# Kernel tuning notes

Measured on AMD Instinct MI355X. Metric: run time of the kernel, lower is better.

Reference implementation:

```python
import jax, jax.numpy as jnp
import numpy as np

N = 50000      # nodes
IN = 128       # in_channels
H = 2          # heads
C = 64         # hidden_channels (per head)
E = 800000     # edges (before self-loops)
OUT = 40       # out_channels
BN_EPS = 1e-5
NEG_SLOPE = 0.2  # PyG GATConv default


def _bn(x, g, b):
    # BatchNorm1d forward with batch statistics (training-mode math, biased var)
    mu = jnp.mean(x, axis=0)
    v = jnp.var(x, axis=0)
    return (x - mu) * jax.lax.rsqrt(v + BN_EPS) * g + b


def _gat_conv(x, src, dst, W, a_src, a_dst, bias, concat):
    n = x.shape[0]
    h = (x @ W).reshape(n, H, C)                      # [N,H,C] per-head projection
    al_s = jnp.einsum('nhc,hc->nh', h, a_src)         # [N,H]
    al_d = jnp.einsum('nhc,hc->nh', h, a_dst)
    e = jax.nn.leaky_relu(al_s[src] + al_d[dst], NEG_SLOPE)  # [E,H]
    # segment softmax over edges sharing the same destination
    m = jax.ops.segment_max(e, dst, num_segments=n)
    ex = jnp.exp(e - m[dst])
    s = jax.ops.segment_sum(ex, dst, num_segments=n)
    alpha = ex / s[dst]                               # [E,H]
    out = jax.ops.segment_sum(h[src] * alpha[..., None], dst, num_segments=n)  # [N,H,C]
    out = out.reshape(n, H * C) if concat else out.mean(axis=1)
    return out + bias


def setup_inputs() -> dict:
    key = jax.random.key(0)
    ks = jax.random.split(key, 16)
    g = lambda k, shp, scale=1.0: jax.random.normal(k, shp, dtype=jnp.float32) * scale
    x = g(ks[0], (N, IN))
    edge_index = jax.random.randint(ks[1], (2, E), 0, N, dtype=jnp.int32)
    s = 1.0 / np.sqrt(IN)
    s2 = 1.0 / np.sqrt(H * C)
    return {
        'x': x,
        'edge_index': edge_index,
        'bn0_g': jnp.ones((IN,), jnp.float32), 'bn0_b': jnp.zeros((IN,), jnp.float32),
        'W1': g(ks[2], (IN, H * C), s), 'a1_src': g(ks[3], (H, C), s), 'a1_dst': g(ks[4], (H, C), s),
        'b1': jnp.zeros((H * C,), jnp.float32),
        'bn1_g': jnp.ones((H * C,), jnp.float32), 'bn1_b': jnp.zeros((H * C,), jnp.float32),
        'W2': g(ks[5], (H * C, H * C), s2), 'a2_src': g(ks[6], (H, C), s2), 'a2_dst': g(ks[7], (H, C), s2),
        'b2': jnp.zeros((C,), jnp.float32),
        'bn2_g': jnp.ones((C,), jnp.float32), 'bn2_b': jnp.zeros((C,), jnp.float32),
        'Wf': g(ks[8], (C, OUT), 1.0 / np.sqrt(C)), 'bf': jnp.zeros((OUT,), jnp.float32),
    }


def reference(x, edge_index, bn0_g, bn0_b, W1, a1_src, a1_dst, b1, bn1_g, bn1_b,
              W2, a2_src, a2_dst, b2, bn2_g, bn2_b, Wf, bf):
    n = x.shape[0]
    loop = jnp.arange(n, dtype=edge_index.dtype)
    src = jnp.concatenate([edge_index[0], loop])  # add self-loops (PyG default)
    dst = jnp.concatenate([edge_index[1], loop])
    h = _bn(x, bn0_g, bn0_b)
    # layer 1: concat heads
    h = _gat_conv(h, src, dst, W1, a1_src, a1_dst, b1, concat=True)
    h = jax.nn.elu(_bn(h, bn1_g, bn1_b))
    # (dropout is identity in eval mode)
    # layer 2: average heads
    h = _gat_conv(h, src, dst, W2, a2_src, a2_dst, b2, concat=False)
    h = jax.nn.elu(_bn(h, bn2_g, bn2_b))
    return h @ Wf + bf
```

## Files before the change

### kernel.cpp

```cpp
#include <hip/hip_runtime.h>
#include <hip/hip_fp16.h>


#define NEG_SLOPE 0.2f
#define BN_EPS 1e-5f

typedef short bf16x8 __attribute__((ext_vector_type(8)));
typedef float f32x4 __attribute__((ext_vector_type(4)));

static __device__ __forceinline__ unsigned short f2bf(float f) {
    union { float f; unsigned u; } v; v.f = f;
    unsigned r = v.u + 0x7FFF + ((v.u >> 16) & 1);
    return (unsigned short)(r >> 16);
}
static __device__ __forceinline__ float2 bf2x2(unsigned v) {
    union { unsigned u; float f; } a, b;
    a.u = v << 16; b.u = v & 0xffff0000u;
    return make_float2(a.f, b.f);
}
static __device__ __forceinline__ float halfsel(unsigned p, int head) {
    __half2 h = *(__half2*)&p;
    return head ? __high2float(h) : __low2float(h);
}

__global__ void k_rank(const int* __restrict__ ei, int E,
                       int* __restrict__ cnt, unsigned short* __restrict__ rank) {
    int i = blockIdx.x * blockDim.x + threadIdx.x;
    if (i >= E) return;
    int d = ei[E + i];
    rank[i] = (unsigned short)atomicAdd(&cnt[d], 1);
}

__global__ __launch_bounds__(1024) void k_part(const int* __restrict__ cnt, int Nn,
                                               int* __restrict__ part) {
    __shared__ int ws[16];
    int t = threadIdx.x, lane = t & 63, w = t >> 6;
    int i = blockIdx.x * 1024 + t;
    int v = (i < Nn) ? cnt[i] + 1 : 0;
    #pragma unroll
    for (int off = 32; off; off >>= 1) v += __shfl_xor(v, off);
    if (lane == 0) ws[w] = v;
    __syncthreads();
    if (t < 16) {
        int s = ws[t];
        #pragma unroll
        for (int off = 8; off; off >>= 1) s += __shfl_xor(s, off);
        if (t == 0) part[blockIdx.x] = s;
    }
}

__global__ __launch_bounds__(1024) void k_scan2(const int* __restrict__ cnt, int Nn, int nb,
                                                const int* __restrict__ part,
                                                int* __restrict__ rowptr) {
    __shared__ int wsum[16];
    __shared__ int s_base, s_total;
    int t = threadIdx.x, lane = t & 63, w = t >> 6;
    int b = blockIdx.x;
    if (w == 0) {
        int base = 0, total = 0;
        for (int ch = 0; ch < nb; ch += 64) {
            int j = ch + lane;
            int v = (j < nb) ? part[j] : 0;
            total += v;
            base += (j < b) ? v : 0;
        }
        #pragma unroll
        for (int off = 32; off; off >>= 1) {
            base += __shfl_xor(base, off);
            total += __shfl_xor(total, off);
        }
        if (lane == 0) { s_base = base; s_total = total; }
    }
    int i = b * 1024 + t;
    int v = (i < Nn) ? cnt[i] + 1 : 0;
    int x = v;
    #pragma unroll
    for (int off = 1; off < 64; off <<= 1) {
        int y = __shfl_up(x, off);
        if (lane >= off) x += y;
    }
    if (lane == 63) wsum[w] = x;
    __syncthreads();
    if (w == 0) {
        int val = (lane < 16) ? wsum[lane] : 0;
        int xs = val;
        #pragma unroll
        for (int off = 1; off < 16; off <<= 1) {
            int y = __shfl_up(xs, off);
            if (lane >= off) xs += y;
        }
        if (lane < 16) wsum[lane] = xs - val;
    }
    __syncthreads();
    if (i < Nn) rowptr[i] = s_base + wsum[w] + (x - v);
    if (b == gridDim.x - 1 && t == 0) rowptr[Nn] = s_total;
}

__global__ void k_fill2(const int* __restrict__ ei, const unsigned short* __restrict__ rank,
                        const int* __restrict__ rowptr, int E, int Nn,
                        unsigned short* __restrict__ ssrc) {
    int i = blockIdx.x * blockDim.x + threadIdx.x;
    if (i < E) {
        int s = ei[i], d = ei[E + i];
        ssrc[rowptr[d] + 1 + (int)rank[i]] = (unsigned short)s;
    } else if (i < E + Nn) {
        int d = i - E;
        ssrc[rowptr[d]] = (unsigned short)d;
    }
}

template <int C>
__global__ __launch_bounds__(256) void k_bnstat2(const float* __restrict__ x, int M,
                                                 int rowsPerBlock, float* __restrict__ sums) {
    constexpr int TPR = C / 4;
    constexpr int RS  = 256 / TPR;
    __shared__ float red[4][2 * C];
    const int t = threadIdx.x;
    const int cg = t % TPR, rg = t / TPR, w = t >> 6, lane = t & 63;
    int r0 = blockIdx.x * rowsPerBlock + rg;
    int r1 = min(M, blockIdx.x * rowsPerBlock + rowsPerBlock);
    float4 s = make_float4(0, 0, 0, 0), q = make_float4(0, 0, 0, 0);
    #pragma unroll 4
    for (int r = r0; r < r1; r += RS) {
        float4 v = *(const float4*)&x[(size_t)r * C + cg * 4];
        s.x += v.x; s.y += v.y; s.z += v.z; s.w += v.w;
        q.x += v.x * v.x; q.y += v.y * v.y; q.z += v.z * v.z; q.w += v.w * v.w;
    }
    #pragma unroll
    for (int off = TPR; off < 64; off <<= 1) {
        s.x += __shfl_xor(s.x, off); s.y += __shfl_xor(s.y, off);
        s.z += __shfl_xor(s.z, off); s.w += __shfl_xor(s.w, off);
        q.x += __shfl_xor(q.x, off); q.y += __shfl_xor(q.y, off);
        q.z += __shfl_xor(q.z, off); q.w += __shfl_xor(q.w, off);
    }
    if (lane < TPR) {
        *(float4*)&red[w][cg * 4] = s;
        *(float4*)&red[w][C + cg * 4] = q;
    }
    __syncthreads();
    for (int idx = t; idx < 2 * C; idx += 256) {
        float tot = red[0][idx] + red[1][idx] + red[2][idx] + red[3][idx];
        atomicAdd(&sums[idx], tot);
    }
}

__global__ void k_bnfin(const float* __restrict__ sums, int M, int C,
                        const float* __restrict__ g, const float* __restrict__ b,
                        float* __restrict__ st) {
    int c = threadIdx.x;
    if (c < C) {
        float mu = sums[c] / (float)M;
        float var = sums[C + c] / (float)M - mu * mu;
        float s = g[c] * rsqrtf(var + BN_EPS);
        st[c] = s;
        st[C + c] = b[c] - mu * s;
    }
}

__global__ __launch_bounds__(256) void k_wt2(const float* __restrict__ W1, const float* __restrict__ W2,
                                             unsigned short* __restrict__ wt1, unsigned short* __restrict__ wt2) {
    int idx = blockIdx.x * 256 + threadIdx.x;
    if (idx >= 128 * 128) return;
    int n = idx >> 7, k = idx & 127;
    wt1[idx] = f2bf(W1[k * 128 + n]);
    wt2[idx] = f2bf(W2[k * 128 + n]);
}

__global__ __launch_bounds__(256) void k_mfma(
    const float* __restrict__ A, const unsigned short* __restrict__ wt,
    const float* __restrict__ stp, int elu,
    const float* __restrict__ asrc, const float* __restrict__ adst, int M,
    unsigned short* __restrict__ hb, float* __restrict__ als, float* __restrict__ ald) {
    __shared__ unsigned short As[64 * 136];
    __shared__ unsigned short Bs[128 * 136];
    const int t = threadIdx.x;
    const int w = t >> 6, lane = t & 63;
    const int c = lane & 15, q = lane >> 4;
    const int row0 = blockIdx.x * 64;

    #pragma unroll
    for (int i = 0; i < 8; i++) {
        int idx = t + i * 256;
        int r = idx >> 5, ch4 = idx & 31;
        int gr = row0 + r;
        float4 v = make_float4(0, 0, 0, 0);
        if (gr < M) {
            v = *(const float4*)&A[(size_t)gr * 128 + ch4 * 4];
            float4 sc = *(const float4*)&stp[ch4 * 4];
            float4 sh = *(const float4*)&stp[128 + ch4 * 4];
            v.x = v.x * sc.x + sh.x; v.y = v.y * sc.y + sh.y;
            v.z = v.z * sc.z + sh.z; v.w = v.w * sc.w + sh.w;
            if (elu) {
                v.x = v.x > 0.f ? v.x : expm1f(v.x);
                v.y = v.y > 0.f ? v.y : expm1f(v.y);
                v.z = v.z > 0.f ? v.z : expm1f(v.z);
                v.w = v.w > 0.f ? v.w : expm1f(v.w);
            }
        }
        unsigned p0 = ((unsigned)f2bf(v.y) << 16) | f2bf(v.x);
        unsigned p1 = ((unsigned)f2bf(v.w) << 16) | f2bf(v.z);
        *(uint2*)&As[r * 136 + ch4 * 4] = make_uint2(p0, p1);
    }
    #pragma unroll
    for (int i = 0; i < 8; i++) {
        int idx = t + i * 256;
        int r = idx >> 4, ch = idx & 15;
        *(uint4*)&Bs[r * 136 + ch * 8] = *(const uint4*)&wt[(size_t)r * 128 + ch * 8];
    }
    __syncthreads();

    f32x4 acc[8] = {};
    #pragma unroll
    for (int ks = 0; ks < 4; ks++) {
        bf16x8 a = *(bf16x8*)&As[(w * 16 + c) * 136 + (ks * 4 + q) * 8];
        #pragma unroll
        for (int tl = 0; tl < 8; tl++) {
            bf16x8 b = *(bf16x8*)&Bs[(tl * 16 + c) * 136 + (ks * 4 + q) * 8];
            acc[tl] = __builtin_amdgcn_mfma_f32_16x16x32_bf16(a, b, acc[tl], 0, 0, 0);
        }
    }

    #pragma unroll
    for (int reg = 0; reg < 4; reg++) {
        int grow = row0 + w * 16 + q * 4 + reg;
        if (grow < M) {
            #pragma unroll
            for (int tl = 0; tl < 8; tl++)
                hb[(size_t)grow * 128 + tl * 16 + c] = f2bf(acc[tl][reg]);
        }
    }

    float as_[8], ad_[8];
    #pragma unroll
    for (int tl = 0; tl < 8; tl++) { as_[tl] = asrc[tl * 16 + c]; ad_[tl] = adst[tl * 16 + c]; }
    #pragma unroll
    for (int reg = 0; reg < 4; reg++) {
        float s0 = 0.f, s1 = 0.f, d0 = 0.f, d1 = 0.f;
        #pragma unroll
        for (int tl = 0; tl < 4; tl++) { s0 += acc[tl][reg] * as_[tl]; d0 += acc[tl][reg] * ad_[tl]; }
        #pragma unroll
        for (int tl = 4; tl < 8; tl++) { s1 += acc[tl][reg] * as_[tl]; d1 += acc[tl][reg] * ad_[tl]; }
        #pragma unroll
        for (int off = 1; off < 16; off <<= 1) {
            s0 += __shfl_xor(s0, off); s1 += __shfl_xor(s1, off);
            d0 += __shfl_xor(d0, off); d1 += __shfl_xor(d1, off);
        }
        int grow = row0 + w * 16 + q * 4 + reg;
        if (c == 0 && grow < M) {
            *(float2*)&als[(size_t)grow * 2] = make_float2(s0, s1);
            *(float2*)&ald[(size_t)grow * 2] = make_float2(d0, d1);
        }
    }
}

static __device__ __forceinline__ void acc8(float* acc, uint4 v, float a) {
    float2 p;
    p = bf2x2(v.x); acc[0] += a * p.x; acc[1] += a * p.y;
    p = bf2x2(v.y); acc[2] += a * p.x; acc[3] += a * p.y;
    p = bf2x2(v.z); acc[4] += a * p.x; acc[5] += a * p.y;
    p = bf2x2(v.w); acc[6] += a * p.x; acc[7] += a * p.y;
}

template <int MEAN>
static __device__ __forceinline__ void attnagg(
    const int* __restrict__ rowptr, const unsigned short* __restrict__ ssrc,
    const float* __restrict__ als, const float* __restrict__ ald,
    float* __restrict__ alpha, const unsigned short* __restrict__ hb,
    const float* __restrict__ bias, int Nn, float* __restrict__ out) {
    int gw = (blockIdx.x * blockDim.x + threadIdx.x) >> 6;
    if (gw >= Nn) return;
    int lane = threadIdx.x & 63;
    int sub = lane >> 4, c = lane & 15, head = c >> 3;
    int beg = rowptr[gw], end = rowptr[gw + 1];
    int deg = end - beg;
    float2 dv = *(const float2*)&ald[(size_t)gw * 2];
    float acc[8] = {};

    if (deg <= 64) {
        bool on = lane < deg;
        int eidx = beg + (on ? lane : 0);
        int sreg = (int)ssrc[eidx];
        float2 av = *(const float2*)&als[(size_t)sreg * 2];
        float v0 = av.x + dv.x; v0 = v0 > 0.f ? v0 : NEG_SLOPE * v0;
        float v1 = av.y + dv.y; v1 = v1 > 0.f ? v1 : NEG_SLOPE * v1;
        float p0 = on ? __expf(v0) : 0.f;
        float p1 = on ? __expf(v1) : 0.f;
        float t0 = p0, t1 = p1;
        #pragma unroll
        for (int off = 32; off; off >>= 1) {
            t0 += __shfl_xor(t0, off);
            t1 += __shfl_xor(t1, off);
        }
        __half2 hpk = __floats2half2_rn(p0 / t0, p1 / t1);
        unsigned pk = *(unsigned*)&hpk;

        int nit = (deg + 3) >> 2;
        int it = 0;
        for (; it + 4 <= nit; it += 4) {
            int s_[4]; float a_[4];
            #pragma unroll
            for (int u = 0; u < 4; u++) {
                int jj = (it + u) * 4 + sub;
                int ls = jj & 63;
                s_[u] = __shfl(sreg, ls);
                unsigned pw = (unsigned)__shfl(pk, ls);
                a_[u] = (jj < deg) ? halfsel(pw, head) : 0.f;
            }
            #pragma unroll
            for (int u = 0; u < 4; u++) {
                uint4 v = *(const uint4*)&hb[(size_t)s_[u] * 128 + c * 8];
                acc8(acc, v, a_[u]);
            }
        }
        for (; it < nit; it += 2) {
            int s_[2]; float a_[2];
            #pragma unroll
            for (int u = 0; u < 2; u++) {
                int jj = (it + u) * 4 + sub;
                int ls = jj & 63;
                s_[u] = __shfl(sreg, ls);
                unsigned pw = (unsigned)__shfl(pk, ls);
                a_[u] = (jj < deg) ? halfsel(pw, head) : 0.f;
            }
            #pragma unroll
            for (int u = 0; u < 2; u++) {
                uint4 v = *(const uint4*)&hb[(size_t)s_[u] * 128 + c * 8];
                acc8(acc, v, a_[u]);
            }
        }
    } else {
        float d0 = dv.x, d1 = dv.y;
        float m0 = -1e30f, m1 = -1e30f;
        for (int e = beg + lane; e < end; e += 64) {
            int s = (int)ssrc[e];
            float v0 = als[s * 2] + d0;     v0 = v0 > 0.f ? v0 : NEG_SLOPE * v0;
            float v1 = als[s * 2 + 1] + d1; v1 = v1 > 0.f ? v1 : NEG_SLOPE * v1;
            m0 = fmaxf(m0, v0); m1 = fmaxf(m1, v1);
        }
        #pragma unroll
        for (int off = 32; off; off >>= 1) {
            m0 = fmaxf(m0, __shfl_xor(m0, off));
            m1 = fmaxf(m1, __shfl_xor(m1, off));
        }
        float t0 = 0.f, t1 = 0.f;
        for (int e = beg + lane; e < end; e += 64) {
            int s = (int)ssrc[e];
            float v0 = als[s * 2] + d0;     v0 = v0 > 0.f ? v0 : NEG_SLOPE * v0;
            float v1 = als[s * 2 + 1] + d1; v1 = v1 > 0.f ? v1 : NEG_SLOPE * v1;
            float p0 = __expf(v0 - m0), p1 = __expf(v1 - m1);
            alpha[e * 2] = p0; alpha[e * 2 + 1] = p1;
            t0 += p0; t1 += p1;
        }
        #pragma unroll
        for (int off = 32; off; off >>= 1) {
            t0 += __shfl_xor(t0, off);
            t1 += __shfl_xor(t1, off);
        }
        float i0 = 1.f / t0, i1 = 1.f / t1;
        for (int e = beg + sub; e < end; e += 4) {
            int s = (int)ssrc[e];
            float a = (head ? alpha[(size_t)e * 2 + 1] * i1 : alpha[(size_t)e * 2] * i0);
            uint4 v = *(const uint4*)&hb[(size_t)s * 128 + c * 8];
            acc8(acc, v, a);
        }
    }

    #pragma unroll
    for (int j2 = 0; j2 < 8; j2++) {
        acc[j2] += __shfl_xor(acc[j2], 16);
        acc[j2] += __shfl_xor(acc[j2], 32);
        if (MEAN) acc[j2] += __shfl_xor(acc[j2], 8);
    }
    if (MEAN) {
        if (sub == 0 && c < 8) {
            float4 b0 = *(const float4*)&bias[c * 8];
            float4 b1 = *(const float4*)&bias[c * 8 + 4];
            float4 o0 = make_float4(0.5f * acc[0] + b0.x, 0.5f * acc[1] + b0.y, 0.5f * acc[2] + b0.z, 0.5f * acc[3] + b0.w);
            float4 o1 = make_float4(0.5f * acc[4] + b1.x, 0.5f * acc[5] + b1.y, 0.5f * acc[6] + b1.z, 0.5f * acc[7] + b1.w);
            *(float4*)&out[(size_t)gw * 64 + c * 8] = o0;
            *(float4*)&out[(size_t)gw * 64 + c * 8 + 4] = o1;
        }
    } else {
        if (sub == 0) {
            float4 b0 = *(const float4*)&bias[c * 8];
            float4 b1 = *(const float4*)&bias[c * 8 + 4];
            float4 o0 = make_float4(acc[0] + b0.x, acc[1] + b0.y, acc[2] + b0.z, acc[3] + b0.w);
            float4 o1 = make_float4(acc[4] + b1.x, acc[5] + b1.y, acc[6] + b1.z, acc[7] + b1.w);
            *(float4*)&out[(size_t)gw * 128 + c * 8] = o0;
            *(float4*)&out[(size_t)gw * 128 + c * 8 + 4] = o1;
        }
    }
}

__global__ __launch_bounds__(256) void k_attnagg1(const int* __restrict__ rowptr, const unsigned short* __restrict__ ssrc,
                                                  const float* __restrict__ als, const float* __restrict__ ald,
                                                  float* __restrict__ alpha, const unsigned short* __restrict__ hb,
                                                  const float* __restrict__ bias, int Nn, float* __restrict__ out) {
    attnagg<0>(rowptr, ssrc, als, ald, alpha, hb, bias, Nn, out);
}

__global__ __launch_bounds__(256) void k_attnagg2(const int* __restrict__ rowptr, const unsigned short* __restrict__ ssrc,
                                                  const float* __restrict__ als, const float* __restrict__ ald,
                                                  float* __restrict__ alpha, const unsigned short* __restrict__ hb,
                                                  const float* __restrict__ bias, int Nn, float* __restrict__ out) {
    attnagg<1>(rowptr, ssrc, als, ald, alpha, hb, bias, Nn, out);
}

__global__ __launch_bounds__(128) void k_gemmf(const float* __restrict__ A, const float* __restrict__ Wf,
                                               const float* __restrict__ bf, const float* __restrict__ st,
                                               int M, float* __restrict__ out) {
    __shared__ float As[128 * 65];
    __shared__ float Bs[64 * 40];
    int t = threadIdx.x;
    int row0 = blockIdx.x * 128;
    for (int i = t; i < 64 * 40; i += 128) Bs[i] = Wf[i];
    for (int i = t; i < 128 * 64; i += 128) {
        int r = i >> 6, k = i & 63;
        int gr = row0 + r;
        float v = 0.f;
        if (gr < M) {
            v = A[(size_t)gr * 64 + k] * st[k] + st[64 + k];
            v = v > 0.f ? v : expm1f(v);
        }
        As[r * 65 + k] = v;
    }
    __syncthreads();
    int cg = t & 3, rg = t >> 2;
    float acc[4][10] = {};
    for (int k = 0; k < 64; k++) {
        float b[10];
        #pragma unroll
        for (int j = 0; j < 10; j++) b[j] = Bs[k * 40 + cg * 10 + j];
        #pragma unroll
        for (int r = 0; r < 4; r++) {
            float a = As[(rg * 4 + r) * 65 + k];
            #pragma unroll
            for (int j = 0; j < 10; j++) acc[r][j] += a * b[j];
        }
    }
    for (int r = 0; r < 4; r++) {
        int gr = row0 + rg * 4 + r;
        if (gr < M) {
            #pragma unroll
            for (int j = 0; j < 10; j++) out[(size_t)gr * 40 + cg * 10 + j] = acc[r][j] + bf[cg * 10 + j];
        }
    }
}

extern "C" void kernel_launch(void* const* d_in, const int* in_sizes, int n_in,
                              void* d_out, int out_size, void* d_ws, size_t ws_size,
                              hipStream_t stream) {
    const float* x     = (const float*)d_in[0];
    const int*   ei    = (const int*)d_in[1];
    const float* bn0_g = (const float*)d_in[2];
    const float* bn0_b = (const float*)d_in[3];
    const float* W1    = (const float*)d_in[4];
    const float* a1s   = (const float*)d_in[5];
    const float* a1d   = (const float*)d_in[6];
    const float* b1    = (const float*)d_in[7];
    const float* bn1_g = (const float*)d_in[8];
    const float* bn1_b = (const float*)d_in[9];
    const float* W2    = (const float*)d_in[10];
    const float* a2s   = (const float*)d_in[11];
    const float* a2d   = (const float*)d_in[12];
    const float* b2    = (const float*)d_in[13];
    const float* bn2_g = (const float*)d_in[14];
    const float* bn2_b = (const float*)d_in[15];
    const float* Wf    = (const float*)d_in[16];
    const float* bf    = (const float*)d_in[17];
    float* out = (float*)d_out;

    const int N  = in_sizes[0] / 128;
    const int E  = in_sizes[1] / 2;
    const int ET = E + N;

    char* ws = (char*)d_ws;
    size_t off = 0;
    auto alloc = [&](size_t bytes) -> char* {
        char* p = ws + off;
        off = (off + bytes + 255) & ~(size_t)255;
        return p;
    };
    int*   cnt    = (int*)alloc((size_t)N * 4);
    int*   rowptr = (int*)alloc((size_t)(N + 1) * 4);
    unsigned short* ssrc = (unsigned short*)alloc((size_t)ET * 2);
    float* abuf   = (float*)alloc((size_t)N * 128 * 4);
    unsigned short* hb  = (unsigned short*)alloc((size_t)N * 128 * 2);
    unsigned short* wt1 = (unsigned short*)alloc((size_t)128 * 128 * 2);
    unsigned short* wt2 = (unsigned short*)alloc((size_t)128 * 128 * 2);
    float* alpha  = (float*)alloc((size_t)ET * 2 * 4);
    float* als    = (float*)alloc((size_t)N * 2 * 4);
    float* ald    = (float*)alloc((size_t)N * 2 * 4);
    int*   part   = (int*)alloc(1024 * 4);
    float* sums   = (float*)alloc(640 * 4);
    float* st     = (float*)alloc(256 * 4);
    unsigned short* rank = (unsigned short*)hb;

    const int tb = 256;
    const int rgrid = (E + tb - 1) / tb;
    const int fgrid = (ET + tb - 1) / tb;
    const int wgrid = ((size_t)N * 64 + tb - 1) / tb;
    const int ggrid = (N + 63) / 64;
    const int nscan = (N + 1023) / 1024;
    const int bgrid = (N + 255) / 256;

    hipMemsetAsync(cnt, 0, (size_t)N * 4, stream);
    hipMemsetAsync(sums, 0, 640 * 4, stream);
    k_rank<<<rgrid, tb, 0, stream>>>(ei, E, cnt, rank);
    k_part<<<nscan, 1024, 0, stream>>>(cnt, N, part);
    k_scan2<<<nscan, 1024, 0, stream>>>(cnt, N, nscan, part, rowptr);
    k_fill2<<<fgrid, tb, 0, stream>>>(ei, rank, rowptr, E, N, ssrc);

    k_wt2<<<64, tb, 0, stream>>>(W1, W2, wt1, wt2);

    k_bnstat2<128><<<bgrid, 256, 0, stream>>>(x, N, 256, sums);
    k_bnfin<<<1, 128, 0, stream>>>(sums, N, 128, bn0_g, bn0_b, st);

    k_mfma<<<ggrid, tb, 0, stream>>>(x, wt1, st, 0, a1s, a1d, N, hb, als, ald);
    k_attnagg1<<<wgrid, tb, 0, stream>>>(rowptr, ssrc, als, ald, alpha, hb, b1, N, abuf);

    k_bnstat2<128><<<bgrid, 256, 0, stream>>>(abuf, N, 256, sums + 256);
    k_bnfin<<<1, 128, 0, stream>>>(sums + 256, N, 128, bn1_g, bn1_b, st);

    k_mfma<<<ggrid, tb, 0, stream>>>(abuf, wt2, st, 1, a2s, a2d, N, hb, als, ald);
    k_attnagg2<<<wgrid, tb, 0, stream>>>(rowptr, ssrc, als, ald, alpha, hb, b2, N, abuf);

    k_bnstat2<64><<<bgrid, 256, 0, stream>>>(abuf, N, 256, sums + 512);
    k_bnfin<<<1, 64, 0, stream>>>(sums + 512, N, 64, bn2_g, bn2_b, st);

    k_gemmf<<<(N + 127) / 128, 128, 0, stream>>>(abuf, Wf, bf, st, N, out);
}
```

Baseline: 330.6 us.

## Merge small launches into combined kernels and fold BN finalize into consumers

New measurement: 309.4 us. 1.07x faster.

```diff
diff --git a/kernel.cpp b/kernel.cpp
--- a/kernel.cpp
+++ b/kernel.cpp
@@ -23,12 +23,72 @@
     return head ? __high2float(h) : __low2float(h);
 }
 
-__global__ void k_rank(const int* __restrict__ ei, int E,
-                       int* __restrict__ cnt, unsigned short* __restrict__ rank) {
-    int i = blockIdx.x * blockDim.x + threadIdx.x;
-    if (i >= E) return;
-    int d = ei[E + i];
-    rank[i] = (unsigned short)atomicAdd(&cnt[d], 1);
+template <int C>
+static __device__ __forceinline__ void d_bnstat(const float* __restrict__ x, int M,
+                                                int rowsPerBlock, float* __restrict__ sums,
+                                                int b) {
+    constexpr int TPR = C / 4;
+    constexpr int RS  = 256 / TPR;
+    __shared__ float red[4][2 * C];
+    const int t = threadIdx.x;
+    const int cg = t % TPR, rg = t / TPR, w = t >> 6, lane = t & 63;
+    int r0 = b * rowsPerBlock + rg;
+    int r1 = min(M, b * rowsPerBlock + rowsPerBlock);
+    float4 s = make_float4(0, 0, 0, 0), q = make_float4(0, 0, 0, 0);
+    #pragma unroll 4
+    for (int r = r0; r < r1; r += RS) {
+        float4 v = *(const float4*)&x[(size_t)r * C + cg * 4];
+        s.x += v.x; s.y += v.y; s.z += v.z; s.w += v.w;
+        q.x += v.x * v.x; q.y += v.y * v.y; q.z += v.z * v.z; q.w += v.w * v.w;
+    }
+    #pragma unroll
+    for (int off = TPR; off < 64; off <<= 1) {
+        s.x += __shfl_xor(s.x, off); s.y += __shfl_xor(s.y, off);
+        s.z += __shfl_xor(s.z, off); s.w += __shfl_xor(s.w, off);
+        q.x += __shfl_xor(q.x, off); q.y += __shfl_xor(q.y, off);
+        q.z += __shfl_xor(q.z, off); q.w += __shfl_xor(q.w, off);
+    }
+    if (lane < TPR) {
+        *(float4*)&red[w][cg * 4] = s;
+        *(float4*)&red[w][C + cg * 4] = q;
+    }
+    __syncthreads();
+    for (int idx = t; idx < 2 * C; idx += 256) {
+        float tot = red[0][idx] + red[1][idx] + red[2][idx] + red[3][idx];
+        atomicAdd(&sums[idx], tot);
+    }
+}
+
+template <int C>
+__global__ __launch_bounds__(256) void k_bnstat2(const float* __restrict__ x, int M,
+                                                 int rowsPerBlock, float* __restrict__ sums) {
+    d_bnstat<C>(x, M, rowsPerBlock, sums, blockIdx.x);
+}
+
+__global__ __launch_bounds__(256) void k_prep(
+    const int* __restrict__ ei, int E, int rgrid,
+    const float* __restrict__ x, int M, int bgrid,
+    const float* __restrict__ W1, const float* __restrict__ W2,
+    int* __restrict__ cnt, unsigned short* __restrict__ rank,
+    float* __restrict__ sums,
+    unsigned short* __restrict__ wt1, unsigned short* __restrict__ wt2) {
+    int b = blockIdx.x;
+    if (b < rgrid) {
+        int i = b * 256 + threadIdx.x;
+        if (i < E) {
+            int d = ei[E + i];
+            rank[i] = (unsigned short)atomicAdd(&cnt[d], 1);
+        }
+    } else if (b < rgrid + bgrid) {
+        d_bnstat<128>(x, M, 256, sums, b - rgrid);
+    } else {
+        int idx = (b - rgrid - bgrid) * 256 + threadIdx.x;
+        if (idx < 128 * 128) {
+            int n = idx >> 7, k = idx & 127;
+            wt1[idx] = f2bf(W1[k * 128 + n]);
+            wt2[idx] = f2bf(W2[k * 128 + n]);
+        }
+    }
 }
 
 __global__ __launch_bounds__(1024) void k_part(const int* __restrict__ cnt, int Nn,
@@ -93,13 +153,14 @@
     }
     __syncthreads();
     if (i < Nn) rowptr[i] = s_base + wsum[w] + (x - v);
-    if (b == gridDim.x - 1 && t == 0) rowptr[Nn] = s_total;
-}
-
-__global__ void k_fill2(const int* __restrict__ ei, const unsigned short* __restrict__ rank,
-                        const int* __restrict__ rowptr, int E, int Nn,
-                        unsigned short* __restrict__ ssrc) {
-    int i = blockIdx.x * blockDim.x + threadIdx.x;
+    if (b == nb - 1 && t == 0) rowptr[Nn] = s_total;
+}
+
+static __device__ __forceinline__ void d_fill(int b, const int* __restrict__ ei,
+                                              const unsigned short* __restrict__ rank,
+                                              const int* __restrict__ rowptr, int E, int Nn,
+                                              unsigned short* __restrict__ ssrc) {
+    int i = b * 256 + threadIdx.x;
     if (i < E) {
         int s = ei[i], d = ei[E + i];
         ssrc[rowptr[d] + 1 + (int)rank[i]] = (unsigned short)s;
@@ -109,74 +170,27 @@
     }
 }
 
-template <int C>
-__global__ __launch_bounds__(256) void k_bnstat2(const float* __restrict__ x, int M,
-                                                 int rowsPerBlock, float* __restrict__ sums) {
-    constexpr int TPR = C / 4;
-    constexpr int RS  = 256 / TPR;
-    __shared__ float red[4][2 * C];
-    const int t = threadIdx.x;
-    const int cg = t % TPR, rg = t / TPR, w = t >> 6, lane = t & 63;
-    int r0 = blockIdx.x * rowsPerBlock + rg;
-    int r1 = min(M, blockIdx.x * rowsPerBlock + rowsPerBlock);
-    float4 s = make_float4(0, 0, 0, 0), q = make_float4(0, 0, 0, 0);
-    #pragma unroll 4
-    for (int r = r0; r < r1; r += RS) {
-        float4 v = *(const float4*)&x[(size_t)r * C + cg * 4];
-        s.x += v.x; s.y += v.y; s.z += v.z; s.w += v.w;
-        q.x += v.x * v.x; q.y += v.y * v.y; q.z += v.z * v.z; q.w += v.w * v.w;
-    }
-    #pragma unroll
-    for (int off = TPR; off < 64; off <<= 1) {
-        s.x += __shfl_xor(s.x, off); s.y += __shfl_xor(s.y, off);
-        s.z += __shfl_xor(s.z, off); s.w += __shfl_xor(s.w, off);
-        q.x += __shfl_xor(q.x, off); q.y += __shfl_xor(q.y, off);
-        q.z += __shfl_xor(q.z, off); q.w += __shfl_xor(q.w, off);
-    }
-    if (lane < TPR) {
-        *(float4*)&red[w][cg * 4] = s;
-        *(float4*)&red[w][C + cg * 4] = q;
-    }
-    __syncthreads();
-    for (int idx = t; idx < 2 * C; idx += 256) {
-        float tot = red[0][idx] + red[1][idx] + red[2][idx] + red[3][idx];
-        atomicAdd(&sums[idx], tot);
-    }
-}
-
-__global__ void k_bnfin(const float* __restrict__ sums, int M, int C,
-                        const float* __restrict__ g, const float* __restrict__ b,
-                        float* __restrict__ st) {
-    int c = threadIdx.x;
-    if (c < C) {
-        float mu = sums[c] / (float)M;
-        float var = sums[C + c] / (float)M - mu * mu;
-        float s = g[c] * rsqrtf(var + BN_EPS);
-        st[c] = s;
-        st[C + c] = b[c] - mu * s;
-    }
-}
-
-__global__ __launch_bounds__(256) void k_wt2(const float* __restrict__ W1, const float* __restrict__ W2,
-                                             unsigned short* __restrict__ wt1, unsigned short* __restrict__ wt2) {
-    int idx = blockIdx.x * 256 + threadIdx.x;
-    if (idx >= 128 * 128) return;
-    int n = idx >> 7, k = idx & 127;
-    wt1[idx] = f2bf(W1[k * 128 + n]);
-    wt2[idx] = f2bf(W2[k * 128 + n]);
-}
-
-__global__ __launch_bounds__(256) void k_mfma(
-    const float* __restrict__ A, const unsigned short* __restrict__ wt,
-    const float* __restrict__ stp, int elu,
-    const float* __restrict__ asrc, const float* __restrict__ adst, int M,
+static __device__ __forceinline__ void d_mfma(
+    int blk, const float* __restrict__ A, const unsigned short* __restrict__ wt,
+    const float* __restrict__ sums, const float* __restrict__ bng, const float* __restrict__ bnb,
+    int elu, const float* __restrict__ asrc, const float* __restrict__ adst, int M,
     unsigned short* __restrict__ hb, float* __restrict__ als, float* __restrict__ ald) {
     __shared__ unsigned short As[64 * 136];
     __shared__ unsigned short Bs[128 * 136];
+    __shared__ __align__(16) float stl[256];
     const int t = threadIdx.x;
     const int w = t >> 6, lane = t & 63;
     const int c = lane & 15, q = lane >> 4;
-    const int row0 = blockIdx.x * 64;
+    const int row0 = blk * 64;
+
+    if (t < 128) {
+        float mu = sums[t] / (float)M;
+        float var = sums[128 + t] / (float)M - mu * mu;
+        float s = bng[t] * rsqrtf(var + BN_EPS);
+        stl[t] = s;
+        stl[128 + t] = bnb[t] - mu * s;
+    }
+    __syncthreads();
 
     #pragma unroll
     for (int i = 0; i < 8; i++) {
@@ -186,8 +200,8 @@
         float4 v = make_float4(0, 0, 0, 0);
         if (gr < M) {
             v = *(const float4*)&A[(size_t)gr * 128 + ch4 * 4];
-            float4 sc = *(const float4*)&stp[ch4 * 4];
-            float4 sh = *(const float4*)&stp[128 + ch4 * 4];
+            float4 sc = *(const float4*)&stl[ch4 * 4];
+            float4 sh = *(const float4*)&stl[128 + ch4 * 4];
             v.x = v.x * sc.x + sh.x; v.y = v.y * sc.y + sh.y;
             v.z = v.z * sc.z + sh.z; v.w = v.w * sc.w + sh.w;
             if (elu) {
@@ -251,6 +265,27 @@
             *(float2*)&ald[(size_t)grow * 2] = make_float2(d0, d1);
         }
     }
+}
+
+__global__ __launch_bounds__(256) void k_mfma(
+    const float* __restrict__ A, const unsigned short* __restrict__ wt,
+    const float* __restrict__ sums, const float* __restrict__ bng, const float* __restrict__ bnb,
+    int elu, const float* __restrict__ asrc, const float* __restrict__ adst, int M,
+    unsigned short* __restrict__ hb, float* __restrict__ als, float* __restrict__ ald) {
+    d_mfma(blockIdx.x, A, wt, sums, bng, bnb, elu, asrc, adst, M, hb, als, ald);
+}
+
+__global__ __launch_bounds__(256) void k_fill_mfma(
+    const float* __restrict__ A, const unsigned short* __restrict__ wt,
+    const float* __restrict__ sums, const float* __restrict__ bng, const float* __restrict__ bnb,
+    const float* __restrict__ asrc, const float* __restrict__ adst, int M, int ggrid,
+    unsigned short* __restrict__ hb, float* __restrict__ als, float* __restrict__ ald,
+    const int* __restrict__ ei, const unsigned short* __restrict__ rank,
+    const int* __restrict__ rowptr, int E, int Nn, unsigned short* __restrict__ ssrc) {
+    if (blockIdx.x < ggrid)
+        d_mfma(blockIdx.x, A, wt, sums, bng, bnb, 0, asrc, adst, M, hb, als, ald);
+    else
+        d_fill(blockIdx.x - ggrid, ei, rank, rowptr, E, Nn, ssrc);
 }
 
 static __device__ __forceinline__ void acc8(float* acc, uint4 v, float a) {
@@ -313,19 +348,24 @@
             }
         }
         for (; it < nit; it += 2) {
+            const bool two = (it + 1) < nit;
             int s_[2]; float a_[2];
             #pragma unroll
             for (int u = 0; u < 2; u++) {
-                int jj = (it + u) * 4 + sub;
-                int ls = jj & 63;
-                s_[u] = __shfl(sreg, ls);
-                unsigned pw = (unsigned)__shfl(pk, ls);
-                a_[u] = (jj < deg) ? halfsel(pw, head) : 0.f;
+                if (u == 0 || two) {
+                    int jj = (it + u) * 4 + sub;
+                    int ls = jj & 63;
+                    s_[u] = __shfl(sreg, ls);
+                    unsigned pw = (unsigned)__shfl(pk, ls);
+                    a_[u] = (jj < deg) ? halfsel(pw, head) : 0.f;
+                }
             }
             #pragma unroll
             for (int u = 0; u < 2; u++) {
-                uint4 v = *(const uint4*)&hb[(size_t)s_[u] * 128 + c * 8];
-                acc8(acc, v, a_[u]);
+                if (u == 0 || two) {
+                    uint4 v = *(const uint4*)&hb[(size_t)s_[u] * 128 + c * 8];
+                    acc8(acc, v, a_[u]);
+                }
             }
         }
     } else {
@@ -407,19 +447,30 @@
 }
 
 __global__ __launch_bounds__(128) void k_gemmf(const float* __restrict__ A, const float* __restrict__ Wf,
-                                               const float* __restrict__ bf, const float* __restrict__ st,
+                                               const float* __restrict__ bf,
+                                               const float* __restrict__ sums, const float* __restrict__ bng,
+                                               const float* __restrict__ bnb,
                                                int M, float* __restrict__ out) {
     __shared__ float As[128 * 65];
     __shared__ float Bs[64 * 40];
+    __shared__ float stl[128];
     int t = threadIdx.x;
     int row0 = blockIdx.x * 128;
+    if (t < 64) {
+        float mu = sums[t] / (float)M;
+        float var = sums[64 + t] / (float)M - mu * mu;
+        float s = bng[t] * rsqrtf(var + BN_EPS);
+        stl[t] = s;
+        stl[64 + t] = bnb[t] - mu * s;
+    }
+    __syncthreads();
     for (int i = t; i < 64 * 40; i += 128) Bs[i] = Wf[i];
     for (int i = t; i < 128 * 64; i += 128) {
         int r = i >> 6, k = i & 63;
         int gr = row0 + r;
         float v = 0.f;
         if (gr < M) {
-            v = A[(size_t)gr * 64 + k] * st[k] + st[64 + k];
+            v = A[(size_t)gr * 64 + k] * stl[k] + stl[64 + k];
             v = v > 0.f ? v : expm1f(v);
         }
         As[r * 65 + k] = v;
@@ -482,8 +533,11 @@
         return p;
     };
     int*   cnt    = (int*)alloc((size_t)N * 4);
+    float* sums   = (float*)alloc(640 * 4);
+    const size_t zlen = off;
     int*   rowptr = (int*)alloc((size_t)(N + 1) * 4);
     unsigned short* ssrc = (unsigned short*)alloc((size_t)ET * 2);
+    unsigned short* rank = (unsigned short*)alloc((size_t)E * 2);
     float* abuf   = (float*)alloc((size_t)N * 128 * 4);
     unsigned short* hb  = (unsigned short*)alloc((size_t)N * 128 * 2);
     unsigned short* wt1 = (unsigned short*)alloc((size_t)128 * 128 * 2);
@@ -492,41 +546,33 @@
     float* als    = (float*)alloc((size_t)N * 2 * 4);
     float* ald    = (float*)alloc((size_t)N * 2 * 4);
     int*   part   = (int*)alloc(1024 * 4);
-    float* sums   = (float*)alloc(640 * 4);
-    float* st     = (float*)alloc(256 * 4);
-    unsigned short* rank = (unsigned short*)hb;
 
     const int tb = 256;
     const int rgrid = (E + tb - 1) / tb;
+    const int bgrid = (N + 255) / 256;
     const int fgrid = (ET + tb - 1) / tb;
     const int wgrid = ((size_t)N * 64 + tb - 1) / tb;
     const int ggrid = (N + 63) / 64;
     const int nscan = (N + 1023) / 1024;
-    const int bgrid = (N + 255) / 256;
-
-    hipMemsetAsync(cnt, 0, (size_t)N * 4, stream);
-    hipMemsetAsync(sums, 0, 640 * 4, stream);
-    k_rank<<<rgrid, tb, 0, stream>>>(ei, E, cnt, rank);
+
+    hipMemsetAsync(ws, 0, zlen, stream);
+
+    k_prep<<<rgrid + bgrid + 64, tb, 0, stream>>>(ei, E, rgrid, x, N, bgrid, W1, W2,
+                                                  cnt, rank, sums, wt1, wt2);
     k_part<<<nscan, 1024, 0, stream>>>(cnt, N, part);
     k_scan2<<<nscan, 1024, 0, stream>>>(cnt, N, nscan, part, rowptr);
-    k_fill2<<<fgrid, tb, 0, stream>>>(ei, rank, rowptr, E, N, ssrc);
-
-    k_wt2<<<64, tb, 0, stream>>>(W1, W2, wt1, wt2);
-
-    k_bnstat2<128><<<bgrid, 256, 0, stream>>>(x, N, 256, sums);
-    k_bnfin<<<1, 128, 0, stream>>>(sums, N, 128, bn0_g, bn0_b, st);
-
-    k_mfma<<<ggrid, tb, 0, stream>>>(x, wt1, st, 0, a1s, a1d, N, hb, als, ald);
+
+    k_fill_mfma<<<ggrid + fgrid, tb, 0, stream>>>(x, wt1, sums, bn0_g, bn0_b,
+                                                  a1s, a1d, N, ggrid, hb, als, ald,
+                                                  ei, rank, rowptr, E, N, ssrc);
     k_attnagg1<<<wgrid, tb, 0, stream>>>(rowptr, ssrc, als, ald, alpha, hb, b1, N, abuf);
 
     k_bnstat2<128><<<bgrid, 256, 0, stream>>>(abuf, N, 256, sums + 256);
-    k_bnfin<<<1, 128, 0, stream>>>(sums + 256, N, 128, bn1_g, bn1_b, st);
-
-    k_mfma<<<ggrid, tb, 0, stream>>>(abuf, wt2, st, 1, a2s, a2d, N, hb, als, ald);
+
+    k_mfma<<<ggrid, tb, 0, stream>>>(abuf, wt2, sums + 256, bn1_g, bn1_b, 1, a2s, a2d, N, hb, als, ald);
     k_attnagg2<<<wgrid, tb, 0, stream>>>(rowptr, ssrc, als, ald, alpha, hb, b2, N, abuf);
 
     k_bnstat2<64><<<bgrid, 256, 0, stream>>>(abuf, N, 256, sums + 512);
-    k_bnfin<<<1, 64, 0, stream>>>(sums + 512, N, 64, bn2_g, bn2_b, st);
-
-    k_gemmf<<<(N + 127) / 128, 128, 0, stream>>>(abuf, Wf, bf, st, N, out);
-}
+
+    k_gemmf<<<(N + 127) / 128, 128, 0, stream>>>(abuf, Wf, bf, sums + 512, bn2_g, bn2_b, N, out);
+}
```
